# Kernel tuning notes

Measured on AMD Instinct MI355X. Metric: run time of the kernel, lower is better.

## Reference

```python
import jax, jax.numpy as jnp
import numpy as np

B, L, H, HKV, D, HID, FFN = 32, 4096, 32, 2, 128, 4096, 13696
ROT = 64  # rotary_dim = kv_channels // 2 (GLM style)
EPS = 1e-5


def setup_inputs() -> dict:
    key = jax.random.key(0)
    ks = jax.random.split(key, 9)
    s = 0.02
    return {
        "hidden_states": jax.random.normal(ks[0], (B, HID), jnp.float32),
        "context_lens": jax.random.randint(ks[1], (B,), 1, L - 1, dtype=jnp.int32),
        "key_cache": jax.random.normal(ks[2], (B, L, HKV, D), jnp.float32),
        "value_cache": jax.random.normal(ks[3], (B, L, HKV, D), jnp.float32),
        "w_ln1": jnp.ones((HID,), jnp.float32),
        "w_ln2": jnp.ones((HID,), jnp.float32),
        "w_qkv": jax.random.normal(ks[4], (HID, H * D + 2 * HKV * D), jnp.float32) * s,
        "b_qkv": jax.random.normal(ks[5], (H * D + 2 * HKV * D,), jnp.float32) * s,
        "w_dense": jax.random.normal(ks[6], (H * D, HID), jnp.float32) * s,
        "w_h4h": jax.random.normal(ks[7], (HID, 2 * FFN), jnp.float32) * s,
        "w_4hh": jax.random.normal(ks[8], (FFN, HID), jnp.float32) * s,
    }


def rmsnorm(x, w):
    v = jnp.mean(x.astype(jnp.float32) ** 2, axis=-1, keepdims=True)
    return (w * (x * jax.lax.rsqrt(v + EPS))).astype(x.dtype)


def apply_rope(x, pos):
    # x: [B, heads, D]; GPT-J interleaved rotary on first ROT dims (glm=True)
    half = ROT // 2
    inv = 1.0 / (10000.0 ** (jnp.arange(half, dtype=jnp.float32) / half))
    f = pos.astype(jnp.float32)[:, None] * inv[None, :]          # [B, half]
    cos, sin = jnp.cos(f)[:, None, :], jnp.sin(f)[:, None, :]    # [B,1,half]
    xr, xp = x[..., :ROT], x[..., ROT:]
    x1, x2 = xr[..., 0::2], xr[..., 1::2]
    rot = jnp.stack([x1 * cos - x2 * sin, x2 * cos + x1 * sin], axis=-1).reshape(xr.shape)
    return jnp.concatenate([rot, xp], axis=-1)


def reference(hidden_states, context_lens, key_cache, value_cache,
              w_ln1, w_ln2, w_qkv, b_qkv, w_dense, w_h4h, w_4hh):
    # input RMSNorm
    ln1 = rmsnorm(hidden_states, w_ln1)
    # fused QKV projection (add_qkv_bias=True)
    qkv = ln1 @ w_qkv + b_qkv
    q, k, v = jnp.split(qkv, [H * D, H * D + HKV * D], axis=-1)
    q = apply_rope(q.reshape(B, H, D), context_lens)
    k = apply_rope(k.reshape(B, HKV, D), context_lens)
    v = v.reshape(B, HKV, D)
    # write new K/V into the paged cache at this token's slot
    kc = key_cache.at[jnp.arange(B), context_lens].set(k)
    vc = value_cache.at[jnp.arange(B), context_lens].set(v)
    # GQA attention: 32 q heads grouped over 2 kv heads
    qg = q.reshape(B, HKV, H // HKV, D)
    scores = jnp.einsum('bghd,blgd->bghl', qg, kc) * (D ** -0.5)
    mask = jnp.arange(L)[None, :] <= context_lens[:, None]       # [B, L]
    scores = jnp.where(mask[:, None, None, :], scores, -jnp.inf)
    p = jax.nn.softmax(scores, axis=-1)
    ctx = jnp.einsum('bghl,blgd->bghd', p, vc).reshape(B, H * D)
    attn_out = ctx @ w_dense                                     # add_bias_linear=False
    x = hidden_states + attn_out                                  # residual pre-LN
    ln2 = rmsnorm(x, w_ln2)
    g, u = jnp.split(ln2 @ w_h4h, 2, axis=-1)
    out = (jax.nn.silu(g) * u) @ w_4hh + x
    return out
```

## Files before the change

### kernel.cpp

```cpp
#include <hip/hip_runtime.h>
#include <hip/hip_bf16.h>

#define B_    32
#define L_    4096
#define H_    32
#define HKV_  2
#define GQ_   16
#define D_    128
#define HID_  4096
#define FFN_  13696
#define NQKV_ 4608
#define ROT_  64
#define EPS_  1e-5f

#define WAVE_POS_ 128
#define NSPLIT_   32

typedef __attribute__((ext_vector_type(8))) __bf16 bf16x8;
typedef __attribute__((ext_vector_type(4))) float  f32x4;

__global__ __launch_bounds__(256) void rmsnorm1_k(const float* __restrict__ x,
                                                  const float* __restrict__ w,
                                                  __bf16* __restrict__ out)
{
    int b = blockIdx.x;
    const float* row = x + (size_t)b * HID_;
    float vals[16];
    float ss = 0.f;
#pragma unroll
    for (int i = 0; i < 16; ++i) {
        vals[i] = row[threadIdx.x + i * 256];
        ss += vals[i] * vals[i];
    }
#pragma unroll
    for (int m = 1; m < 64; m <<= 1) ss += __shfl_xor(ss, m);
    __shared__ float wred[4];
    if ((threadIdx.x & 63) == 0) wred[threadIdx.x >> 6] = ss;
    __syncthreads();
    ss = wred[0] + wred[1] + wred[2] + wred[3];
    float rs = rsqrtf(ss / HID_ + EPS_);
#pragma unroll
    for (int i = 0; i < 16; ++i) {
        int idx = threadIdx.x + i * 256;
        out[(size_t)b * HID_ + idx] = (__bf16)(w[idx] * vals[i] * rs);
    }
}

template<int K, int N, int KSPLIT>
__global__ __launch_bounds__(256) void gemm16(const __bf16* __restrict__ A,
                                              const float* __restrict__ W,
                                              float* __restrict__ Cp)
{
    static_assert(K % 32 == 0, "K");
    const int lane = threadIdx.x & 63;
    const int wid  = threadIdx.x >> 6;
    const int n0   = blockIdx.x * 32;
    const int r    = lane & 15;
    const int g4   = lane >> 4;
    constexpr int ksteps = K / 32;
    constexpr int nch    = KSPLIT * 4;
    const int cid = blockIdx.y * 4 + wid;
    const int s0  = (ksteps * cid) / nch;
    const int s1  = (ksteps * (cid + 1)) / nch;

    f32x4 acc00 = {0.f,0.f,0.f,0.f}, acc01 = acc00, acc10 = acc00, acc11 = acc00;
    const float*  wp  = W + n0 + r;
    const __bf16* a0p = A + (size_t)r * K;
    const __bf16* a1p = A + (size_t)(r + 16) * K;

#pragma unroll 2
    for (int s = s0; s < s1; ++s) {
        const int k0 = s * 32 + g4 * 8;
        const float* wk = wp + (size_t)k0 * N;
        bf16x8 b0, b1;
#pragma unroll
        for (int j = 0; j < 8; ++j) {
            b0[j] = (__bf16)wk[(size_t)j * N];
            b1[j] = (__bf16)wk[(size_t)j * N + 16];
        }
        bf16x8 av0 = *(const bf16x8*)(a0p + k0);
        bf16x8 av1 = *(const bf16x8*)(a1p + k0);
        acc00 = __builtin_amdgcn_mfma_f32_16x16x32_bf16(av0, b0, acc00, 0, 0, 0);
        acc10 = __builtin_amdgcn_mfma_f32_16x16x32_bf16(av1, b0, acc10, 0, 0, 0);
        acc01 = __builtin_amdgcn_mfma_f32_16x16x32_bf16(av0, b1, acc01, 0, 0, 0);
        acc11 = __builtin_amdgcn_mfma_f32_16x16x32_bf16(av1, b1, acc11, 0, 0, 0);
    }

    __shared__ float red[4][32][32];
#pragma unroll
    for (int i = 0; i < 4; ++i) {
        red[wid][g4 * 4 + i][r]           = acc00[i];
        red[wid][g4 * 4 + i][16 + r]      = acc01[i];
        red[wid][16 + g4 * 4 + i][r]      = acc10[i];
        red[wid][16 + g4 * 4 + i][16 + r] = acc11[i];
    }
    __syncthreads();
    for (int idx = threadIdx.x; idx < 1024; idx += 256) {
        int row = idx >> 5, col = idx & 31;
        float v = red[0][row][col] + red[1][row][col] + red[2][row][col] + red[3][row][col];
        Cp[((size_t)blockIdx.y * 32 + row) * N + n0 + col] = v;
    }
}

__global__ __launch_bounds__(256) void qkv_epi_k(const float* __restrict__ part,
                                                 const float* __restrict__ bias,
                                                 const int* __restrict__ ctxl,
                                                 __bf16* __restrict__ qbf,
                                                 float* __restrict__ knew,
                                                 float* __restrict__ vnew)
{
    __shared__ float rowv[NQKV_];
    int b = blockIdx.x;
    for (int i = threadIdx.x; i < NQKV_; i += 256) {
        float v = bias[i];
#pragma unroll
        for (int p = 0; p < 4; ++p) v += part[((size_t)p * B_ + b) * NQKV_ + i];
        rowv[i] = v;
    }
    __syncthreads();
    int pos = ctxl[b];
    const float qscale = 0.08838834764831845f;
    for (int i = threadIdx.x; i < HID_; i += 256) {
        int d = i & 127;
        float o;
        if (d < ROT_) {
            int t = d >> 1;
            float inv = powf(10000.f, -(float)t * (1.0f / 32.0f));
            float f = (float)pos * inv;
            float sv, cv; sincosf(f, &sv, &cv);
            float x1 = rowv[i & ~1], x2 = rowv[i | 1];
            o = (d & 1) ? (x2 * cv + x1 * sv) : (x1 * cv - x2 * sv);
        } else o = rowv[i];
        qbf[(size_t)b * HID_ + i] = (__bf16)(o * qscale);
    }
    for (int i = threadIdx.x; i < HKV_ * D_; i += 256) {
        int d = i & 127;
        float o;
        if (d < ROT_) {
            int t = d >> 1;
            float inv = powf(10000.f, -(float)t * (1.0f / 32.0f));
            float f = (float)pos * inv;
            float sv, cv; sincosf(f, &sv, &cv);
            float x1 = rowv[HID_ + (i & ~1)], x2 = rowv[HID_ + (i | 1)];
            o = (d & 1) ? (x2 * cv + x1 * sv) : (x1 * cv - x2 * sv);
        } else o = rowv[HID_ + i];
        knew[(size_t)b * HKV_ * D_ + i] = o;
        vnew[(size_t)b * HKV_ * D_ + i] = rowv[HID_ + HKV_ * D_ + i];
    }
}

__global__ __launch_bounds__(256) void attn_k(const float* __restrict__ kc,
                                              const float* __restrict__ vc,
                                              const float* __restrict__ knew,
                                              const float* __restrict__ vnew,
                                              const __bf16* __restrict__ qbf,
                                              const int* __restrict__ ctxl,
                                              float* __restrict__ part)
{
    const int bg  = blockIdx.x;
    const int b   = bg >> 1, g = bg & 1;
    const int wid = threadIdx.x >> 6;
    const int split = blockIdx.y * 4 + wid;
    const int ctx = ctxl[b];
    const int p0  = split * WAVE_POS_;
    __shared__ __bf16 plds_all[4][16][40];
    if (p0 > ctx) return;
    const int pend = min(p0 + WAVE_POS_ - 1, ctx);
    const int lane = threadIdx.x & 63;
    const int r = lane & 15, g4 = lane >> 4;

    bf16x8 qf[4];
    {
        const __bf16* qp = qbf + (size_t)b * HID_ + (g * GQ_ + r) * D_ + g4 * 8;
#pragma unroll
        for (int kk = 0; kk < 4; ++kk) qf[kk] = *(const bf16x8*)(qp + kk * 32);
    }
    f32x4 acc[8];
#pragma unroll
    for (int dt = 0; dt < 8; ++dt) acc[dt] = (f32x4){0.f,0.f,0.f,0.f};
    float m_run[4], l_run[4];
#pragma unroll
    for (int i = 0; i < 4; ++i) { m_run[i] = -1e30f; l_run[i] = 0.f; }

    auto plds = plds_all[wid];
    const float* kbase = kc + ((size_t)b * L_ * HKV_ + g) * D_;
    const float* vbase = vc + ((size_t)b * L_ * HKV_ + g) * D_;
    const float* knp = knew + (size_t)(b * HKV_ + g) * D_;
    const float* vnp = vnew + (size_t)(b * HKV_ + g) * D_;

    for (int pc = p0; pc <= pend; pc += 32) {
        f32x4 sf[2];
#pragma unroll
        for (int pt = 0; pt < 2; ++pt) {
            int pos = pc + pt * 16 + r;
            const float* krow = (pos == ctx) ? knp : kbase + (size_t)pos * (HKV_ * D_);
            f32x4 s = {0.f,0.f,0.f,0.f};
#pragma unroll
            for (int kk = 0; kk < 4; ++kk) {
                const float* kp = krow + kk * 32 + g4 * 8;
                bf16x8 kf;
#pragma unroll
                for (int j = 0; j < 8; ++j) kf[j] = (__bf16)kp[j];
                s = __builtin_amdgcn_mfma_f32_16x16x32_bf16(qf[kk], kf, s, 0, 0, 0);
            }
            sf[pt] = s;
        }
#pragma unroll
        for (int pt = 0; pt < 2; ++pt) {
            int pos = pc + pt * 16 + r;
            if (pos > ctx) {
#pragma unroll
                for (int i = 0; i < 4; ++i) sf[pt][i] = -1e30f;
            }
        }
#pragma unroll
        for (int i = 0; i < 4; ++i) {
            float mv = fmaxf(sf[0][i], sf[1][i]);
            mv = fmaxf(mv, __shfl_xor(mv, 1));
            mv = fmaxf(mv, __shfl_xor(mv, 2));
            mv = fmaxf(mv, __shfl_xor(mv, 4));
            mv = fmaxf(mv, __shfl_xor(mv, 8));
            float mnew = fmaxf(m_run[i], mv);
            float sc = __expf(m_run[i] - mnew);
            l_run[i] *= sc;
            m_run[i] = mnew;
#pragma unroll
            for (int dt = 0; dt < 8; ++dt) acc[dt][i] *= sc;
        }
#pragma unroll
        for (int pt = 0; pt < 2; ++pt) {
#pragma unroll
            for (int i = 0; i < 4; ++i) {
                float e = __expf(sf[pt][i] - m_run[i]);
                l_run[i] += e;
                plds[g4 * 4 + i][pt * 16 + r] = (__bf16)e;
            }
        }
        asm volatile("s_waitcnt lgkmcnt(0)" ::: "memory");
        bf16x8 pa = *(const bf16x8*)&plds[r][g4 * 8];
        const float* vrows[8];
#pragma unroll
        for (int j = 0; j < 8; ++j) {
            int pos = pc + g4 * 8 + j;
            vrows[j] = (pos == ctx) ? vnp : vbase + (size_t)pos * (HKV_ * D_);
        }
#pragma unroll
        for (int dt = 0; dt < 8; ++dt) {
            bf16x8 vf;
#pragma unroll
            for (int j = 0; j < 8; ++j) vf[j] = (__bf16)vrows[j][dt * 16 + r];
            acc[dt] = __builtin_amdgcn_mfma_f32_16x16x32_bf16(pa, vf, acc[dt], 0, 0, 0);
        }
        asm volatile("s_waitcnt lgkmcnt(0)" ::: "memory");
    }
#pragma unroll
    for (int i = 0; i < 4; ++i) {
        float lv = l_run[i];
        lv += __shfl_xor(lv, 1);
        lv += __shfl_xor(lv, 2);
        lv += __shfl_xor(lv, 4);
        lv += __shfl_xor(lv, 8);
        l_run[i] = lv;
    }
    float* pb = part + ((size_t)bg * NSPLIT_ + split) * 16 * 130;
#pragma unroll
    for (int dt = 0; dt < 8; ++dt)
#pragma unroll
        for (int i = 0; i < 4; ++i)
            pb[(g4 * 4 + i) * 130 + dt * 16 + r] = acc[dt][i];
    if (r == 0) {
#pragma unroll
        for (int i = 0; i < 4; ++i) {
            pb[(g4 * 4 + i) * 130 + 128] = m_run[i];
            pb[(g4 * 4 + i) * 130 + 129] = l_run[i];
        }
    }
}

__global__ __launch_bounds__(256) void attn_comb_k(const float* __restrict__ part,
                                                   const int* __restrict__ ctxl,
                                                   __bf16* __restrict__ ctxb)
{
    int bg = blockIdx.x;
    int b = bg >> 1, g = bg & 1;
    int ctx = ctxl[b];
    int ns = ctx / WAVE_POS_ + 1;
    const float* pb = part + (size_t)bg * NSPLIT_ * 16 * 130;
    __shared__ float Wgt[NSPLIT_][16];
    __shared__ float Dn[16];
    int t = threadIdx.x;
    if (t < 16) {
        int h = t;
        float M = -1e30f;
        for (int s = 0; s < ns; ++s) M = fmaxf(M, pb[(s * 16 + h) * 130 + 128]);
        float den = 0.f;
        for (int s = 0; s < ns; ++s) {
            float w = __expf(pb[(s * 16 + h) * 130 + 128] - M);
            Wgt[s][h] = w;
            den += w * pb[(s * 16 + h) * 130 + 129];
        }
        Dn[h] = den;
    }
    __syncthreads();
    int h = t >> 4, d0 = (t & 15) * 8;
    float o[8];
#pragma unroll
    for (int j = 0; j < 8; ++j) o[j] = 0.f;
    for (int s = 0; s < ns; ++s) {
        float w = Wgt[s][h];
        const float* ap = pb + (s * 16 + h) * 130 + d0;
#pragma unroll
        for (int j = 0; j < 8; ++j) o[j] += w * ap[j];
    }
    float inv = 1.f / Dn[h];
#pragma unroll
    for (int j = 0; j < 8; ++j)
        ctxb[(size_t)b * HID_ + (g * GQ_ + h) * D_ + d0 + j] = (__bf16)(o[j] * inv);
}

__global__ __launch_bounds__(256) void dense_epi_k(const float* __restrict__ hidden,
                                                   const float* __restrict__ partd,
                                                   const float* __restrict__ wln2,
                                                   float* __restrict__ xout,
                                                   __bf16* __restrict__ a2)
{
    __shared__ float xr[HID_];
    int b = blockIdx.x;
    float ss = 0.f;
    for (int i = threadIdx.x; i < HID_; i += 256) {
        float v = hidden[(size_t)b * HID_ + i];
#pragma unroll
        for (int p = 0; p < 4; ++p) v += partd[((size_t)p * B_ + b) * HID_ + i];
        xr[i] = v;
        ss += v * v;
        xout[(size_t)b * HID_ + i] = v;
    }
#pragma unroll
    for (int m = 1; m < 64; m <<= 1) ss += __shfl_xor(ss, m);
    __shared__ float wred[4];
    if ((threadIdx.x & 63) == 0) wred[threadIdx.x >> 6] = ss;
    __syncthreads();
    ss = wred[0] + wred[1] + wred[2] + wred[3];
    float rs = rsqrtf(ss / HID_ + EPS_);
    for (int i = threadIdx.x; i < HID_; i += 256)
        a2[(size_t)b * HID_ + i] = (__bf16)(wln2[i] * xr[i] * rs);
}

__global__ __launch_bounds__(256) void act_k(const float* __restrict__ gu,
                                             __bf16* __restrict__ act)
{
    int i = blockIdx.x * 256 + threadIdx.x;
    int b = blockIdx.y;
    if (i < FFN_) {
        float gv = gu[(size_t)b * 2 * FFN_ + i];
        float uv = gu[(size_t)b * 2 * FFN_ + FFN_ + i];
        float s = gv / (1.f + __expf(-gv));
        act[(size_t)b * FFN_ + i] = (__bf16)(s * uv);
    }
}

__global__ __launch_bounds__(256) void out_epi_k(const float* __restrict__ x,
                                                 const float* __restrict__ part4,
                                                 float* __restrict__ out)
{
    int i = blockIdx.x * 256 + threadIdx.x;
    float v = x[i];
#pragma unroll
    for (int p = 0; p < 4; ++p) v += part4[(size_t)p * (B_ * HID_) + i];
    out[i] = v;
}

extern "C" void kernel_launch(void* const* d_in, const int* in_sizes, int n_in,
                              void* d_out, int out_size, void* d_ws, size_t ws_size,
                              hipStream_t stream)
{
    const float* hidden  = (const float*)d_in[0];
    const int*   ctxl    = (const int*)d_in[1];
    const float* kcache  = (const float*)d_in[2];
    const float* vcache  = (const float*)d_in[3];
    const float* w_ln1   = (const float*)d_in[4];
    const float* w_ln2   = (const float*)d_in[5];
    const float* w_qkv   = (const float*)d_in[6];
    const float* b_qkv   = (const float*)d_in[7];
    const float* w_dense = (const float*)d_in[8];
    const float* w_h4h   = (const float*)d_in[9];
    const float* w_4hh   = (const float*)d_in[10];
    float* out = (float*)d_out;

    char* ws = (char*)d_ws;
    size_t off = 0;
    auto alloc = [&](size_t bytes) -> void* {
        void* p = ws + off;
        off += (bytes + 255) & ~(size_t)255;
        return p;
    };
    __bf16* a0    = (__bf16*)alloc((size_t)B_ * HID_ * 2);
    float*  partq = (float*) alloc((size_t)4 * B_ * NQKV_ * 4);
    __bf16* qbf   = (__bf16*)alloc((size_t)B_ * HID_ * 2);
    float*  knew  = (float*) alloc((size_t)B_ * HKV_ * D_ * 4);
    float*  vnew  = (float*) alloc((size_t)B_ * HKV_ * D_ * 4);
    float*  apart = (float*) alloc((size_t)B_ * HKV_ * NSPLIT_ * 16 * 130 * 4);
    __bf16* ctxb  = (__bf16*)alloc((size_t)B_ * HID_ * 2);
    float*  partd = (float*) alloc((size_t)4 * B_ * HID_ * 4);
    float*  xbuf  = (float*) alloc((size_t)B_ * HID_ * 4);
    __bf16* a2    = (__bf16*)alloc((size_t)B_ * HID_ * 2);
    float*  gu    = (float*) alloc((size_t)B_ * 2 * FFN_ * 4);
    __bf16* actb  = (__bf16*)alloc((size_t)B_ * FFN_ * 2);
    float*  part4 = (float*) alloc((size_t)4 * B_ * HID_ * 4);
    (void)ws_size; (void)in_sizes; (void)n_in; (void)out_size;

    hipLaunchKernelGGL(rmsnorm1_k, dim3(B_), dim3(256), 0, stream, hidden, w_ln1, a0);
    hipLaunchKernelGGL((gemm16<HID_, NQKV_, 4>), dim3(NQKV_ / 32, 4), dim3(256), 0, stream, a0, w_qkv, partq);
    hipLaunchKernelGGL(qkv_epi_k, dim3(B_), dim3(256), 0, stream, partq, b_qkv, ctxl, qbf, knew, vnew);
    hipLaunchKernelGGL(attn_k, dim3(B_ * HKV_, NSPLIT_ / 4), dim3(256), 0, stream,
                       kcache, vcache, knew, vnew, qbf, ctxl, apart);
    hipLaunchKernelGGL(attn_comb_k, dim3(B_ * HKV_), dim3(256), 0, stream, apart, ctxl, ctxb);
    hipLaunchKernelGGL((gemm16<HID_, HID_, 4>), dim3(HID_ / 32, 4), dim3(256), 0, stream, ctxb, w_dense, partd);
    hipLaunchKernelGGL(dense_epi_k, dim3(B_), dim3(256), 0, stream, hidden, partd, w_ln2, xbuf, a2);
    hipLaunchKernelGGL((gemm16<HID_, 2 * FFN_, 1>), dim3(2 * FFN_ / 32, 1), dim3(256), 0, stream, a2, w_h4h, gu);
    hipLaunchKernelGGL(act_k, dim3((FFN_ + 255) / 256, B_), dim3(256), 0, stream, gu, actb);
    hipLaunchKernelGGL((gemm16<FFN_, HID_, 4>), dim3(HID_ / 32, 4), dim3(256), 0, stream, actb, w_4hh, part4);
    hipLaunchKernelGGL(out_epi_k, dim3(B_ * HID_ / 256), dim3(256), 0, stream, xbuf, part4, out);
}
```

Before: 316.6 us.

## Stage GEMM weights through LDS with prefetch, vectorize K loads, precompute RoPE tables

The skinny GEMM now reads each fp32 weight tile with coalesced float4 loads, prefetched one k-step ahead in registers. It transposes the tile into a per-wave LDS buffer as bf16 before the MFMA fragment reads, replacing the old strided scalar loads. The attention kernel loads K rows as two float4 instead of eight scalar reads and adds sched_barriers around its LDS waits. The QKV epilogue computes the 32 RoPE sin/cos values once per block in shared memory instead of once per element. The GEMM change adds LDS traffic and extra waitcnt/sched barriers per step, which could serialize the loop.

```diff
diff --git a/kernel.cpp b/kernel.cpp
--- a/kernel.cpp
+++ b/kernel.cpp
@@ -52,38 +52,61 @@
                                               float* __restrict__ Cp)
 {
     static_assert(K % 32 == 0, "K");
+    constexpr int ksteps = K / 32;
+    constexpr int nch    = KSPLIT * 4;
     const int lane = threadIdx.x & 63;
     const int wid  = threadIdx.x >> 6;
     const int n0   = blockIdx.x * 32;
     const int r    = lane & 15;
     const int g4   = lane >> 4;
-    constexpr int ksteps = K / 32;
-    constexpr int nch    = KSPLIT * 4;
-    const int cid = blockIdx.y * 4 + wid;
-    const int s0  = (ksteps * cid) / nch;
-    const int s1  = (ksteps * (cid + 1)) / nch;
+    const int cid  = blockIdx.y * 4 + wid;
+    const int s0   = (ksteps * cid) / nch;
+    const int s1   = (ksteps * (cid + 1)) / nch;
+
+    const int kk_b = lane >> 3;
+    const int c4   = (lane & 7) * 4;
+
+    __shared__ __bf16 tiles[4][32][40];
+    __bf16 (*tile)[40] = tiles[wid];
 
     f32x4 acc00 = {0.f,0.f,0.f,0.f}, acc01 = acc00, acc10 = acc00, acc11 = acc00;
-    const float*  wp  = W + n0 + r;
     const __bf16* a0p = A + (size_t)r * K;
     const __bf16* a1p = A + (size_t)(r + 16) * K;
 
-#pragma unroll 2
+    float4 pf[4];
+    auto issue = [&](int s) {
+        const float* wk = W + (size_t)(s * 32 + kk_b) * N + n0 + c4;
+#pragma unroll
+        for (int it = 0; it < 4; ++it)
+            pf[it] = *(const float4*)(wk + (size_t)(it * 8) * N);
+    };
+
+    if (s0 < s1) issue(s0);
     for (int s = s0; s < s1; ++s) {
-        const int k0 = s * 32 + g4 * 8;
-        const float* wk = wp + (size_t)k0 * N;
-        bf16x8 b0, b1;
-#pragma unroll
-        for (int j = 0; j < 8; ++j) {
-            b0[j] = (__bf16)wk[(size_t)j * N];
-            b1[j] = (__bf16)wk[(size_t)j * N + 16];
-        }
-        bf16x8 av0 = *(const bf16x8*)(a0p + k0);
-        bf16x8 av1 = *(const bf16x8*)(a1p + k0);
+        float4 cur[4];
+#pragma unroll
+        for (int it = 0; it < 4; ++it) cur[it] = pf[it];
+        if (s + 1 < s1) issue(s + 1);
+#pragma unroll
+        for (int it = 0; it < 4; ++it) {
+            int kk = it * 8 + kk_b;
+            tile[c4 + 0][kk] = (__bf16)cur[it].x;
+            tile[c4 + 1][kk] = (__bf16)cur[it].y;
+            tile[c4 + 2][kk] = (__bf16)cur[it].z;
+            tile[c4 + 3][kk] = (__bf16)cur[it].w;
+        }
+        asm volatile("s_waitcnt lgkmcnt(0)" ::: "memory");
+        __builtin_amdgcn_sched_barrier(0);
+        bf16x8 b0  = *(const bf16x8*)&tile[r][g4 * 8];
+        bf16x8 b1  = *(const bf16x8*)&tile[r + 16][g4 * 8];
+        bf16x8 av0 = *(const bf16x8*)(a0p + s * 32 + g4 * 8);
+        bf16x8 av1 = *(const bf16x8*)(a1p + s * 32 + g4 * 8);
         acc00 = __builtin_amdgcn_mfma_f32_16x16x32_bf16(av0, b0, acc00, 0, 0, 0);
         acc10 = __builtin_amdgcn_mfma_f32_16x16x32_bf16(av1, b0, acc10, 0, 0, 0);
         acc01 = __builtin_amdgcn_mfma_f32_16x16x32_bf16(av0, b1, acc01, 0, 0, 0);
         acc11 = __builtin_amdgcn_mfma_f32_16x16x32_bf16(av1, b1, acc11, 0, 0, 0);
+        asm volatile("s_waitcnt lgkmcnt(0)" ::: "memory");
+        __builtin_amdgcn_sched_barrier(0);
     }
 
     __shared__ float red[4][32][32];
@@ -110,7 +133,16 @@
                                                  float* __restrict__ vnew)
 {
     __shared__ float rowv[NQKV_];
+    __shared__ float cs[32], sn[32];
     int b = blockIdx.x;
+    int pos = ctxl[b];
+    if (threadIdx.x < 32) {
+        int t = threadIdx.x;
+        float inv = powf(10000.f, -(float)t * (1.0f / 32.0f));
+        float f = (float)pos * inv;
+        float sv, cv; sincosf(f, &sv, &cv);
+        cs[t] = cv; sn[t] = sv;
+    }
     for (int i = threadIdx.x; i < NQKV_; i += 256) {
         float v = bias[i];
 #pragma unroll
@@ -118,16 +150,13 @@
         rowv[i] = v;
     }
     __syncthreads();
-    int pos = ctxl[b];
     const float qscale = 0.08838834764831845f;
     for (int i = threadIdx.x; i < HID_; i += 256) {
         int d = i & 127;
         float o;
         if (d < ROT_) {
             int t = d >> 1;
-            float inv = powf(10000.f, -(float)t * (1.0f / 32.0f));
-            float f = (float)pos * inv;
-            float sv, cv; sincosf(f, &sv, &cv);
+            float cv = cs[t], sv = sn[t];
             float x1 = rowv[i & ~1], x2 = rowv[i | 1];
             o = (d & 1) ? (x2 * cv + x1 * sv) : (x1 * cv - x2 * sv);
         } else o = rowv[i];
@@ -138,9 +167,7 @@
         float o;
         if (d < ROT_) {
             int t = d >> 1;
-            float inv = powf(10000.f, -(float)t * (1.0f / 32.0f));
-            float f = (float)pos * inv;
-            float sv, cv; sincosf(f, &sv, &cv);
+            float cv = cs[t], sv = sn[t];
             float x1 = rowv[HID_ + (i & ~1)], x2 = rowv[HID_ + (i | 1)];
             o = (d & 1) ? (x2 * cv + x1 * sv) : (x1 * cv - x2 * sv);
         } else o = rowv[HID_ + i];
@@ -197,10 +224,10 @@
             f32x4 s = {0.f,0.f,0.f,0.f};
 #pragma unroll
             for (int kk = 0; kk < 4; ++kk) {
-                const float* kp = krow + kk * 32 + g4 * 8;
-                bf16x8 kf;
-#pragma unroll
-                for (int j = 0; j < 8; ++j) kf[j] = (__bf16)kp[j];
+                const float4* kp = (const float4*)(krow + kk * 32 + g4 * 8);
+                float4 fa = kp[0], fb = kp[1];
+                bf16x8 kf = { (__bf16)fa.x, (__bf16)fa.y, (__bf16)fa.z, (__bf16)fa.w,
+                              (__bf16)fb.x, (__bf16)fb.y, (__bf16)fb.z, (__bf16)fb.w };
                 s = __builtin_amdgcn_mfma_f32_16x16x32_bf16(qf[kk], kf, s, 0, 0, 0);
             }
             sf[pt] = s;
@@ -237,6 +264,7 @@
             }
         }
         asm volatile("s_waitcnt lgkmcnt(0)" ::: "memory");
+        __builtin_amdgcn_sched_barrier(0);
         bf16x8 pa = *(const bf16x8*)&plds[r][g4 * 8];
         const float* vrows[8];
 #pragma unroll
@@ -252,6 +280,7 @@
             acc[dt] = __builtin_amdgcn_mfma_f32_16x16x32_bf16(pa, vf, acc[dt], 0, 0, 0);
         }
         asm volatile("s_waitcnt lgkmcnt(0)" ::: "memory");
+        __builtin_amdgcn_sched_barrier(0);
     }
 #pragma unroll
     for (int i = 0; i < 4; ++i) {
```

Measured after the change: 300.5 us. 1.05x faster.
